# Optimization experiments

Measured on AMD Instinct MI355X. Metric: run time of the kernel, lower is better.

Reference implementation:

```python
import jax, jax.numpy as jnp
import numpy as np

NUM_HEADS = 8
HEAD_DIM = 32
ATTN_DIM = NUM_HEADS * HEAD_DIM  # 256
WINDOW_SIZES = (7, 5)
DILATIONS = (1, 2)
SCALE_FACTORS = (2, 4)


def conv1x1(x, W, b):
    # x: [B, C, H, W], W: [O, C], b: [O]
    return jnp.einsum('bchw,oc->bohw', x, W) + b[None, :, None, None]


def gather_neighbors(x, window, dilation):
    """Zero-padded dilated neighborhood gather.
    x: [B, C, h, w] -> neighbors [B, C, K, h, w], valid mask [K, h, w] (K = window**2)."""
    B, C, h, w = x.shape
    pad = dilation * (window // 2)
    xp = jnp.pad(x, ((0, 0), (0, 0), (pad, pad), (pad, pad)))
    mp = jnp.pad(jnp.ones((h, w), dtype=bool), ((pad, pad), (pad, pad)))
    neigh, masks = [], []
    for i in range(window):
        for j in range(window):
            dy, dx = dilation * i, dilation * j
            neigh.append(xp[:, :, dy:dy + h, dx:dx + w])
            masks.append(mp[dy:dy + h, dx:dx + w])
    return jnp.stack(neigh, axis=2), jnp.stack(masks, axis=0)


def align_to_query_grid(t, Hq, Wq, sf):
    """Repeat coarse-lattice candidates onto the fine query grid via anchor indexing."""
    y = jnp.minimum(jnp.arange(Hq) // sf, t.shape[-2] - 1)
    x = jnp.minimum(jnp.arange(Wq) // sf, t.shape[-1] - 1)
    return jnp.take(jnp.take(t, y, axis=-2), x, axis=-1)


def _forward(query, mems, Wq, bq, Wks, bks, Wvs, bvs, Wfuse, bfuse):
    B, _, Hq, Wq_ = query.shape
    q = conv1x1(query, Wq, bq)                                  # [B, attn, Hq, Wq]
    qh = q.reshape(B, NUM_HEADS, HEAD_DIM, Hq, Wq_)             # [B, n, d, H, W]
    scale = HEAD_DIM ** -0.5
    outs = []
    for s, mem in enumerate(mems):
        k = conv1x1(mem, Wks[s], bks[s])                        # [B, attn, hm, wm]
        v = conv1x1(mem, Wvs[s], bvs[s])
        kn, mask = gather_neighbors(k, WINDOW_SIZES[s], DILATIONS[s])  # [B, attn, K, hm, wm]
        vn, _ = gather_neighbors(v, WINDOW_SIZES[s], DILATIONS[s])
        K = kn.shape[2]
        hm, wm = kn.shape[-2:]
        kn = kn.reshape(B, NUM_HEADS, HEAD_DIM, K, hm, wm).transpose(0, 1, 3, 2, 4, 5)  # [B,n,K,d,hm,wm]
        vn = vn.reshape(B, NUM_HEADS, HEAD_DIM, K, hm, wm).transpose(0, 1, 3, 2, 4, 5)
        kn = align_to_query_grid(kn, Hq, Wq_, SCALE_FACTORS[s])  # [B,n,K,d,Hq,Wq]
        vn = align_to_query_grid(vn, Hq, Wq_, SCALE_FACTORS[s])
        mask_f = align_to_query_grid(mask, Hq, Wq_, SCALE_FACTORS[s])  # [K,Hq,Wq]
        scores = jnp.einsum('bndhw,bnkdhw->bnkhw', qh, kn) * scale
        neg = jnp.finfo(scores.dtype).min
        scores = jnp.where(mask_f[None, None], scores, neg)
        attn = jax.nn.softmax(scores, axis=2)                    # over K candidates
        o = jnp.einsum('bnkhw,bnkdhw->bndhw', attn, vn)
        outs.append(o.reshape(B, ATTN_DIM, Hq, Wq_))
    fused = jnp.concatenate(outs, axis=1)                        # [B, S*attn, Hq, Wq]
    return conv1x1(fused, Wfuse, bfuse)                          # [B, attn, Hq, Wq]


def setup_inputs() -> dict:
    key = jax.random.key(0)
    ks = jax.random.split(key, 16)
    std = 0.02
    inp = {
        'query': jax.random.normal(ks[0], (2, 256, 64, 64), jnp.float32),
        'mem0': jax.random.normal(ks[1], (2, 384, 32, 32), jnp.float32),
        'mem1': jax.random.normal(ks[2], (2, 768, 16, 16), jnp.float32),
        'Wq': jax.random.normal(ks[3], (ATTN_DIM, 256), jnp.float32) * std,
        'bq': jnp.zeros((ATTN_DIM,), jnp.float32),
        'Wk0': jax.random.normal(ks[4], (ATTN_DIM, 384), jnp.float32) * std,
        'bk0': jnp.zeros((ATTN_DIM,), jnp.float32),
        'Wv0': jax.random.normal(ks[5], (ATTN_DIM, 384), jnp.float32) * std,
        'bv0': jnp.zeros((ATTN_DIM,), jnp.float32),
        'Wk1': jax.random.normal(ks[6], (ATTN_DIM, 768), jnp.float32) * std,
        'bk1': jnp.zeros((ATTN_DIM,), jnp.float32),
        'Wv1': jax.random.normal(ks[7], (ATTN_DIM, 768), jnp.float32) * std,
        'bv1': jnp.zeros((ATTN_DIM,), jnp.float32),
        'Wfuse': jax.random.normal(ks[8], (ATTN_DIM, 2 * ATTN_DIM), jnp.float32) * std,
        'bfuse': jnp.zeros((ATTN_DIM,), jnp.float32),
    }
    return inp


def reference(query, mem0, mem1, Wq, bq, Wk0, bk0, Wv0, bv0, Wk1, bk1, Wv1, bv1, Wfuse, bfuse):
    return _forward(query, (mem0, mem1), Wq, bq, (Wk0, Wk1), (bk0, bk1), (Wv0, Wv1), (bv0, bv1), Wfuse, bfuse)
```

## Files before the change

kernel.cpp:

```cpp
#include <hip/hip_runtime.h>
#include <math.h>

typedef unsigned short u16;
typedef unsigned int u32;
typedef __attribute__((ext_vector_type(8))) short bf16x8;
typedef __attribute__((ext_vector_type(4))) float f32x4;

__device__ __forceinline__ u16 f2bf(float x) {
    u32 b = __builtin_bit_cast(u32, x);
    b += 0x7FFFu + ((b >> 16) & 1u);
    return (u16)(b >> 16);
}
__device__ __forceinline__ float bf2f(u16 u) {
    u32 b = ((u32)u) << 16;
    return __builtin_bit_cast(float, b);
}

__device__ __forceinline__ size_t sw_unit(int row, int c, int CC) {
    int slot = (c & 63) >> 3;
    return ((size_t)((row >> 7) * CC + (c >> 6)) << 10)
         + (size_t)((row & 127) << 3) + (size_t)(slot ^ (row & 7));
}

__device__ void prep_x(const float* __restrict__ X, int C, int HW, int bl, int PT,
                       u16* __restrict__ dh) {
    __shared__ float Xt[64][65];
    const int t = threadIdx.x;
    const int pt = bl % PT, ct = bl / PT;
    const int p0 = pt * 64, c0 = ct * 64;
    const int b = p0 / HW, hw0 = p0 % HW;
    #pragma unroll
    for (int i = 0; i < 16; i++) {
        int r = (t >> 6) + i * 4;
        Xt[r][t & 63] = X[(size_t)(b * C + c0 + r) * HW + hw0 + (t & 63)];
    }
    __syncthreads();
    const int CC = C >> 6;
    #pragma unroll
    for (int it = 0; it < 2; it++) {
        int id = t + it * 256;
        int px = id >> 3, sl = id & 7;
        bf16x8 hv;
        #pragma unroll
        for (int j = 0; j < 8; j++)
            hv[j] = (short)f2bf(Xt[sl * 8 + j][px]);
        size_t unit = sw_unit(p0 + px, c0 + sl * 8, CC);
        *(bf16x8*)(dh + unit * 8) = hv;
    }
}

__device__ void prep_w(const float* __restrict__ W, int C, int bl,
                       u16* __restrict__ dh, u16* __restrict__ dl, bool wlo) {
    const int t = threadIdx.x;
    const int ot = bl & 3, cc = bl >> 2;
    const int o0 = ot * 64, c0 = cc * 64;
    const int CC = C >> 6;
    #pragma unroll
    for (int it = 0; it < 2; it++) {
        int id = t + it * 256;
        int ol = id >> 3, sl = id & 7;
        int o = o0 + ol, c = c0 + sl * 8;
        const float* wp = W + (size_t)o * C + c;
        float4 a = *(const float4*)wp;
        float4 b2 = *(const float4*)(wp + 4);
        float xs[8] = {a.x, a.y, a.z, a.w, b2.x, b2.y, b2.z, b2.w};
        bf16x8 hv, lv;
        #pragma unroll
        for (int j = 0; j < 8; j++) {
            u16 h = f2bf(xs[j]);
            hv[j] = (short)h;
            lv[j] = (short)f2bf(xs[j] - bf2f(h));
        }
        size_t unit = sw_unit(o, c, CC);
        *(bf16x8*)(dh + unit * 8) = hv;
        if (wlo) *(bf16x8*)(dl + unit * 8) = lv;
    }
}

#define OFF_WQ 0
#define OFF_WK0 65536
#define OFF_WV0 163840
#define OFF_WK1 262144
#define OFF_WV1 458752
#define OFF_WFUSE 655360

__global__ __launch_bounds__(256) void prep_k(
    const float* __restrict__ query, const float* __restrict__ mem0, const float* __restrict__ mem1,
    const float* __restrict__ Wq, const float* __restrict__ Wk0, const float* __restrict__ Wv0,
    const float* __restrict__ Wk1, const float* __restrict__ Wv1, const float* __restrict__ Wfuse,
    u16* Xq_hi, u16* Xm0_hi, u16* Xm1_hi, u16* Whi, u16* Wlo)
{
    const int bx = blockIdx.x;
    if (bx < 512)      prep_x(query, 256, 4096, bx,       128, Xq_hi);
    else if (bx < 704) prep_x(mem0,  384, 1024, bx - 512,  32, Xm0_hi);
    else if (bx < 800) prep_x(mem1,  768,  256, bx - 704,   8, Xm1_hi);
    else {
        int r = bx - 800;
        if (r < 16)       prep_w(Wq,    256, r,       Whi + OFF_WQ,    Wlo, false);
        else if (r < 40)  prep_w(Wk0,   384, r - 16,  Whi + OFF_WK0,   Wlo, false);
        else if (r < 64)  prep_w(Wv0,   384, r - 40,  Whi + OFF_WV0,   Wlo, false);
        else if (r < 112) prep_w(Wk1,   768, r - 64,  Whi + OFF_WK1,   Wlo, false);
        else if (r < 160) prep_w(Wv1,   768, r - 112, Whi + OFF_WV1,   Wlo, false);
        else              prep_w(Wfuse, 512, r - 160, Whi + OFF_WFUSE, Wlo + OFF_WFUSE, true);
    }
}

template<int TERMS, bool OUT16>
__device__ __forceinline__ void gemm_core(
    const u16* __restrict__ Ahi, const u16* __restrict__ Alo,
    const u16* __restrict__ Bhi, const float* __restrict__ bias,
    void* __restrict__ Y, int CC, int am, int bn, u16* smem)
{
    const int t = threadIdx.x, lane = t & 63, w = t >> 6;
    const int wr = w >> 1, wc = w & 1;
    const int l15 = lane & 15;

    f32x4 acc[4][4];
    #pragma unroll
    for (int a = 0; a < 4; a++)
        #pragma unroll
        for (int b2 = 0; b2 < 4; b2++)
            acc[a][b2] = (f32x4){0.f, 0.f, 0.f, 0.f};

    bf16x8 stg[TERMS + 1][4];
    {
        const size_t aoff = ((size_t)(am * CC)) << 13;
        const size_t boff = ((size_t)(bn * CC)) << 13;
        #pragma unroll
        for (int it = 0; it < 4; it++) {
            const size_t o = (size_t)(t + it * 256) * 8;
            stg[0][it] = *(const bf16x8*)(Ahi + aoff + o);
            if constexpr (TERMS == 2) stg[1][it] = *(const bf16x8*)(Alo + aoff + o);
            stg[TERMS][it] = *(const bf16x8*)(Bhi + boff + o);
        }
    }

    for (int ck = 0; ck < CC; ck++) {
        __syncthreads();
        #pragma unroll
        for (int p = 0; p <= TERMS; p++)
            #pragma unroll
            for (int it = 0; it < 4; it++)
                *(bf16x8*)(smem + p * 8192 + (size_t)(t + it * 256) * 8) = stg[p][it];
        __syncthreads();

        {
            const int cn = (ck + 1 < CC) ? ck + 1 : ck;
            const size_t aoff = ((size_t)(am * CC + cn)) << 13;
            const size_t boff = ((size_t)(bn * CC + cn)) << 13;
            #pragma unroll
            for (int it = 0; it < 4; it++) {
                const size_t o = (size_t)(t + it * 256) * 8;
                stg[0][it] = *(const bf16x8*)(Ahi + aoff + o);
                if constexpr (TERMS == 2) stg[1][it] = *(const bf16x8*)(Alo + aoff + o);
                stg[TERMS][it] = *(const bf16x8*)(Bhi + boff + o);
            }
        }

        #pragma unroll
        for (int kk = 0; kk < 2; kk++) {
            bf16x8 ah[4], al[4], bh[4];
            #pragma unroll
            for (int tr = 0; tr < 4; tr++) {
                int row = wr * 64 + tr * 16 + l15;
                int off = row * 64 + (((kk * 4 + (lane >> 4)) ^ (row & 7)) << 3);
                ah[tr] = *(const bf16x8*)(smem + off);
                if constexpr (TERMS == 2) al[tr] = *(const bf16x8*)(smem + 8192 + off);
            }
            #pragma unroll
            for (int tc = 0; tc < 4; tc++) {
                int row = wc * 64 + tc * 16 + l15;
                int off = row * 64 + (((kk * 4 + (lane >> 4)) ^ (row & 7)) << 3);
                bh[tc] = *(const bf16x8*)(smem + TERMS * 8192 + off);
            }
            #pragma unroll
            for (int tr = 0; tr < 4; tr++)
                #pragma unroll
                for (int tc = 0; tc < 4; tc++) {
                    acc[tr][tc] = __builtin_amdgcn_mfma_f32_16x16x32_bf16(ah[tr], bh[tc], acc[tr][tc], 0, 0, 0);
                    if constexpr (TERMS == 2)
                        acc[tr][tc] = __builtin_amdgcn_mfma_f32_16x16x32_bf16(al[tr], bh[tc], acc[tr][tc], 0, 0, 0);
                }
        }
    }

    if (OUT16) {
        u16* Y16 = (u16*)Y;
        float bv[4];
        #pragma unroll
        for (int tc = 0; tc < 4; tc++)
            bv[tc] = bias[bn * 128 + wc * 64 + tc * 16 + l15];
        #pragma unroll
        for (int tr = 0; tr < 4; tr++) {
            #pragma unroll
            for (int i = 0; i < 4; i++) {
                int rp = am * 128 + wr * 64 + tr * 16 + ((lane >> 4) << 2) + i;
                u16* yr = Y16 + (size_t)rp * 256 + bn * 128 + wc * 64 + l15;
                #pragma unroll
                for (int tc = 0; tc < 4; tc++)
                    yr[tc * 16] = f2bf(acc[tr][tc][i] + bv[tc]);
            }
        }
    } else {
        float* Yf = (float*)Y;
        #pragma unroll
        for (int tr = 0; tr < 4; tr++) {
            #pragma unroll
            for (int i = 0; i < 4; i++) {
                int o = am * 128 + wr * 64 + tr * 16 + ((lane >> 4) << 2) + i;
                float bv = bias[o];
                #pragma unroll
                for (int tc = 0; tc < 4; tc++) {
                    int pcol = bn * 128 + wc * 64 + tc * 16 + l15;
                    Yf[(size_t)((pcol >> 12) * 256 + o) * 4096 + (pcol & 4095)] = acc[tr][tc][i] + bv;
                }
            }
        }
    }
}

__global__ __launch_bounds__(256) void projmm_k(
    const u16* __restrict__ Xq_hi, const u16* __restrict__ Xm0_hi,
    const u16* __restrict__ Xm1_hi, const u16* __restrict__ Whi,
    const float* __restrict__ bq, const float* __restrict__ bk0, const float* __restrict__ bv0,
    const float* __restrict__ bk1, const float* __restrict__ bv1,
    u16* qT, u16* k0T, u16* v0T, u16* k1T, u16* v1T)
{
    __shared__ u16 smem[16384];
    const int bx = blockIdx.x;
    if (bx < 128) {
        gemm_core<1, true>(Xq_hi, nullptr, Whi + OFF_WQ, bq, (void*)qT, 4, bx >> 1, bx & 1, smem);
    } else if (bx < 192) {
        const int r = bx - 128, am = r >> 2, bnn = r & 3;
        if (bnn < 2) gemm_core<1, true>(Xm0_hi, nullptr, Whi + OFF_WK0, bk0, (void*)k0T, 6, am, bnn, smem);
        else         gemm_core<1, true>(Xm0_hi, nullptr, Whi + OFF_WV0, bv0, (void*)v0T, 6, am, bnn - 2, smem);
    } else {
        const int r = bx - 192, am = r >> 2, bnn = r & 3;
        if (bnn < 2) gemm_core<1, true>(Xm1_hi, nullptr, Whi + OFF_WK1, bk1, (void*)k1T, 12, am, bnn, smem);
        else         gemm_core<1, true>(Xm1_hi, nullptr, Whi + OFF_WV1, bv1, (void*)v1T, 12, am, bnn - 2, smem);
    }
}

__global__ __launch_bounds__(256) void fusemm_k(
    const u16* __restrict__ Whi, const u16* __restrict__ Wlo,
    const u16* __restrict__ fhi, const float* __restrict__ bfuse, float* out)
{
    __shared__ u16 smem[24576];
    const int bx = blockIdx.x;
    gemm_core<2, false>(Whi + OFF_WFUSE, Wlo + OFF_WFUSE, fhi, bfuse, (void*)out,
                        8, bx & 1, bx >> 1, smem);
}

template<int SCALE>
__device__ __forceinline__ void attn_mfma(
    const u16* __restrict__ qT, const u16* __restrict__ kT,
    const u16* __restrict__ vT, u16* __restrict__ fhi,
    int b, int n, int ty, int tx, int lane, u16* s_lds)
{
    constexpr int HM = SCALE ? 16 : 32;
    const int qy0 = ty * 4, qx0 = tx * 4;
    const int ay0 = SCALE ? (qy0 >> 2) : (qy0 >> 1);
    const int ax0 = SCALE ? (qx0 >> 2) : (qx0 >> 1);
    const int l15 = lane & 15, kg = lane >> 4;

    const int pA = (b * 64 + qy0 + (l15 >> 2)) * 64 + qx0 + (l15 & 3);
    const bf16x8 qf = *(const bf16x8*)(qT + (size_t)pA * 256 + n * 32 + kg * 8);

    f32x4 s[4];
    #pragma unroll
    for (int t = 0; t < 4; t++) {
        const int cand = t * 16 + l15;
        const int wy = cand >> 3, wx = cand & 7;
        const int my = SCALE ? (ay0 + (wy - 2) * 2) : (ay0 - 3 + wy);
        const int mx = SCALE ? (ax0 + (wx - 2) * 2) : (ax0 - 3 + wx);
        const int myc = min(max(my, 0), HM - 1), mxc = min(max(mx, 0), HM - 1);
        const bf16x8 kf = *(const bf16x8*)(kT + (size_t)((b * HM + myc) * HM + mxc) * 256 + n * 32 + kg * 8);
        s[t] = __builtin_amdgcn_mfma_f32_16x16x32_bf16(qf, kf, (f32x4){0.f, 0.f, 0.f, 0.f}, 0, 0, 0);
    }

    const float scl = 0.17677669529663687f;
    float sv[4][4];
    #pragma unroll
    for (int t = 0; t < 4; t++) {
        const int cand = t * 16 + l15;
        const int wy = cand >> 3, wx = cand & 7;
        const int my = SCALE ? (ay0 + (wy - 2) * 2) : (ay0 - 3 + wy);
        const int mx = SCALE ? (ax0 + (wx - 2) * 2) : (ax0 - 3 + wx);
        const bool inb = (my >= 0) && (my < HM) && (mx >= 0) && (mx < HM);
        #pragma unroll
        for (int i = 0; i < 4; i++) {
            bool ok;
            if (SCALE) {
                ok = inb && (wy < 5) && (wx < 5);
            } else {
                const int r = kg * 4 + i;
                const int dy2 = (r >> 2) >> 1, dx2 = (r & 3) >> 1;
                ok = inb && ((u32)(wy - dy2) <= 6u) && ((u32)(wx - dx2) <= 6u);
            }
            sv[t][i] = ok ? s[t][i] * scl : -1e30f;
        }
    }

    float linv[4];
    #pragma unroll
    for (int i = 0; i < 4; i++) {
        float m = fmaxf(fmaxf(sv[0][i], sv[1][i]), fmaxf(sv[2][i], sv[3][i]));
        #pragma unroll
        for (int dd = 1; dd < 16; dd <<= 1) m = fmaxf(m, __shfl_xor(m, dd, 64));
        float l = 0.f;
        #pragma unroll
        for (int t = 0; t < 4; t++) { sv[t][i] = __expf(sv[t][i] - m); l += sv[t][i]; }
        #pragma unroll
        for (int dd = 1; dd < 16; dd <<= 1) l += __shfl_xor(l, dd, 64);
        linv[i] = 1.f / l;
    }

    #pragma unroll
    for (int t = 0; t < 4; t++)
        #pragma unroll
        for (int i = 0; i < 4; i++)
            s_lds[(kg * 4 + i) * 68 + t * 16 + l15] = f2bf(sv[t][i]);
    __syncthreads();

    f32x4 o[2] = {(f32x4){0.f,0.f,0.f,0.f}, (f32x4){0.f,0.f,0.f,0.f}};
    #pragma unroll
    for (int h = 0; h < 2; h++) {
        const bf16x8 pa = *(const bf16x8*)(s_lds + l15 * 68 + h * 32 + kg * 8);
        #pragma unroll
        for (int c = 0; c < 2; c++) {
            bf16x8 vf;
            #pragma unroll
            for (int j = 0; j < 8; j++) {
                const int cand = h * 32 + kg * 8 + j;
                const int wy = cand >> 3, wx = cand & 7;
                int my = SCALE ? (ay0 + (wy - 2) * 2) : (ay0 - 3 + wy);
                int mx = SCALE ? (ax0 + (wx - 2) * 2) : (ax0 - 3 + wx);
                my = min(max(my, 0), HM - 1); mx = min(max(mx, 0), HM - 1);
                vf[j] = (short)vT[(size_t)((b * HM + my) * HM + mx) * 256 + n * 32 + c * 16 + l15];
            }
            o[c] = __builtin_amdgcn_mfma_f32_16x16x32_bf16(pa, vf, o[c], 0, 0, 0);
        }
    }

    #pragma unroll
    for (int c = 0; c < 2; c++) {
        #pragma unroll
        for (int i = 0; i < 4; i++) {
            const int r = kg * 4 + i;
            const int p = (b * 64 + qy0 + (r >> 2)) * 64 + qx0 + (r & 3);
            const int ch = (SCALE ? 256 : 0) + n * 32 + c * 16 + l15;
            fhi[sw_unit(p, ch, 8) * 8 + (ch & 7)] = f2bf(o[c][i] * linv[i]);
        }
    }
}

__global__ __launch_bounds__(256) void attn_k(
    const u16* __restrict__ qT,
    const u16* __restrict__ k0T, const u16* __restrict__ v0T,
    const u16* __restrict__ k1T, const u16* __restrict__ v1T,
    u16* __restrict__ fhi)
{
    __shared__ u16 s_lds[4][16 * 68];
    const int t = threadIdx.x, w = t >> 6, lane = t & 63;
    const int bx = blockIdx.x;
    const int sc = bx >> 10;
    const int tile = (bx & 1023) * 4 + w;
    const int b = tile >> 11, n = (tile >> 8) & 7;
    const int ty = (tile >> 4) & 15, tx = tile & 15;
    if (sc == 0) attn_mfma<0>(qT, k0T, v0T, fhi, b, n, ty, tx, lane, s_lds[w]);
    else         attn_mfma<1>(qT, k1T, v1T, fhi, b, n, ty, tx, lane, s_lds[w]);
}

extern "C" void kernel_launch(void* const* d_in, const int* in_sizes, int n_in,
                              void* d_out, int out_size, void* d_ws, size_t ws_size,
                              hipStream_t stream)
{
    const float* query = (const float*)d_in[0];
    const float* mem0  = (const float*)d_in[1];
    const float* mem1  = (const float*)d_in[2];
    const float* Wq    = (const float*)d_in[3];  const float* bq    = (const float*)d_in[4];
    const float* Wk0   = (const float*)d_in[5];  const float* bk0   = (const float*)d_in[6];
    const float* Wv0   = (const float*)d_in[7];  const float* bv0   = (const float*)d_in[8];
    const float* Wk1   = (const float*)d_in[9];  const float* bk1   = (const float*)d_in[10];
    const float* Wv1   = (const float*)d_in[11]; const float* bv1   = (const float*)d_in[12];
    const float* Wfuse = (const float*)d_in[13]; const float* bfuse = (const float*)d_in[14];
    float* out = (float*)d_out;

    char* ws = (char*)d_ws;
    u16* qT       = (u16*)(ws + 0);
    u16* k0T      = (u16*)(ws + 8388608);
    u16* v0T      = (u16*)(ws + 10485760);
    u16* k1T      = (u16*)(ws + 12582912);
    u16* v1T      = (u16*)(ws + 13107200);
    u16* Whi      = (u16*)(ws + 13631488);
    u16* Wlo      = (u16*)(ws + 15204352);
    u16* Xm0_hi   = (u16*)(ws + 16777216);
    u16* Xm1_hi   = (u16*)(ws + 19922944);
    u16* Xq_hi    = (u16*)(ws + 21495808);
    u16* fhi      = Xq_hi;

    prep_k<<<dim3(992), 256, 0, stream>>>(
        query, mem0, mem1, Wq, Wk0, Wv0, Wk1, Wv1, Wfuse,
        Xq_hi, Xm0_hi, Xm1_hi, Whi, Wlo);

    projmm_k<<<dim3(208), 256, 0, stream>>>(
        Xq_hi, Xm0_hi, Xm1_hi, Whi,
        bq, bk0, bv0, bk1, bv1, qT, k0T, v0T, k1T, v1T);

    attn_k<<<dim3(2048), 256, 0, stream>>>(qT, k0T, v0T, k1T, v1T, fhi);

    fusemm_k<<<dim3(128), 256, 0, stream>>>(Whi, Wlo, fhi, bfuse, out);
}
```

Baseline: 56.04 us.

## Drop split-bf16 low term in fuse GEMM and retile it to 64-row blocks

The fuse projection no longer uses a hi/lo split of the weights, so it runs one bf16 MFMA per tile instead of two and stops loading and storing the low-part weights. The fuse GEMM also becomes its own kernel with 64x128 output tiles and 256 blocks instead of 128, to fill more compute units and use less LDS per block. This lowers the accuracy of the final projection, which now runs at plain bf16 precision and may come closer to the tolerance limit.

```diff
diff --git a/kernel.cpp b/kernel.cpp
--- a/kernel.cpp
+++ b/kernel.cpp
@@ -50,7 +50,7 @@
 }
 
 __device__ void prep_w(const float* __restrict__ W, int C, int bl,
-                       u16* __restrict__ dh, u16* __restrict__ dl, bool wlo) {
+                       u16* __restrict__ dh) {
     const int t = threadIdx.x;
     const int ot = bl & 3, cc = bl >> 2;
     const int o0 = ot * 64, c0 = cc * 64;
@@ -64,16 +64,12 @@
         float4 a = *(const float4*)wp;
         float4 b2 = *(const float4*)(wp + 4);
         float xs[8] = {a.x, a.y, a.z, a.w, b2.x, b2.y, b2.z, b2.w};
-        bf16x8 hv, lv;
-        #pragma unroll
-        for (int j = 0; j < 8; j++) {
-            u16 h = f2bf(xs[j]);
-            hv[j] = (short)h;
-            lv[j] = (short)f2bf(xs[j] - bf2f(h));
-        }
+        bf16x8 hv;
+        #pragma unroll
+        for (int j = 0; j < 8; j++)
+            hv[j] = (short)f2bf(xs[j]);
         size_t unit = sw_unit(o, c, CC);
         *(bf16x8*)(dh + unit * 8) = hv;
-        if (wlo) *(bf16x8*)(dl + unit * 8) = lv;
     }
 }
 
@@ -88,7 +84,7 @@
     const float* __restrict__ query, const float* __restrict__ mem0, const float* __restrict__ mem1,
     const float* __restrict__ Wq, const float* __restrict__ Wk0, const float* __restrict__ Wv0,
     const float* __restrict__ Wk1, const float* __restrict__ Wv1, const float* __restrict__ Wfuse,
-    u16* Xq_hi, u16* Xm0_hi, u16* Xm1_hi, u16* Whi, u16* Wlo)
+    u16* Xq_hi, u16* Xm0_hi, u16* Xm1_hi, u16* Whi)
 {
     const int bx = blockIdx.x;
     if (bx < 512)      prep_x(query, 256, 4096, bx,       128, Xq_hi);
@@ -96,20 +92,19 @@
     else if (bx < 800) prep_x(mem1,  768,  256, bx - 704,   8, Xm1_hi);
     else {
         int r = bx - 800;
-        if (r < 16)       prep_w(Wq,    256, r,       Whi + OFF_WQ,    Wlo, false);
-        else if (r < 40)  prep_w(Wk0,   384, r - 16,  Whi + OFF_WK0,   Wlo, false);
-        else if (r < 64)  prep_w(Wv0,   384, r - 40,  Whi + OFF_WV0,   Wlo, false);
-        else if (r < 112) prep_w(Wk1,   768, r - 64,  Whi + OFF_WK1,   Wlo, false);
-        else if (r < 160) prep_w(Wv1,   768, r - 112, Whi + OFF_WV1,   Wlo, false);
-        else              prep_w(Wfuse, 512, r - 160, Whi + OFF_WFUSE, Wlo + OFF_WFUSE, true);
-    }
-}
-
-template<int TERMS, bool OUT16>
+        if (r < 16)       prep_w(Wq,    256, r,       Whi + OFF_WQ);
+        else if (r < 40)  prep_w(Wk0,   384, r - 16,  Whi + OFF_WK0);
+        else if (r < 64)  prep_w(Wv0,   384, r - 40,  Whi + OFF_WV0);
+        else if (r < 112) prep_w(Wk1,   768, r - 64,  Whi + OFF_WK1);
+        else if (r < 160) prep_w(Wv1,   768, r - 112, Whi + OFF_WV1);
+        else              prep_w(Wfuse, 512, r - 160, Whi + OFF_WFUSE);
+    }
+}
+
 __device__ __forceinline__ void gemm_core(
-    const u16* __restrict__ Ahi, const u16* __restrict__ Alo,
-    const u16* __restrict__ Bhi, const float* __restrict__ bias,
-    void* __restrict__ Y, int CC, int am, int bn, u16* smem)
+    const u16* __restrict__ Ahi, const u16* __restrict__ Bhi,
+    const float* __restrict__ bias, u16* __restrict__ Y,
+    int CC, int am, int bn, u16* smem)
 {
     const int t = threadIdx.x, lane = t & 63, w = t >> 6;
     const int wr = w >> 1, wc = w & 1;
@@ -122,7 +117,7 @@
         for (int b2 = 0; b2 < 4; b2++)
             acc[a][b2] = (f32x4){0.f, 0.f, 0.f, 0.f};
 
-    bf16x8 stg[TERMS + 1][4];
+    bf16x8 stg[2][4];
     {
         const size_t aoff = ((size_t)(am * CC)) << 13;
         const size_t boff = ((size_t)(bn * CC)) << 13;
@@ -130,15 +125,14 @@
         for (int it = 0; it < 4; it++) {
             const size_t o = (size_t)(t + it * 256) * 8;
             stg[0][it] = *(const bf16x8*)(Ahi + aoff + o);
-            if constexpr (TERMS == 2) stg[1][it] = *(const bf16x8*)(Alo + aoff + o);
-            stg[TERMS][it] = *(const bf16x8*)(Bhi + boff + o);
+            stg[1][it] = *(const bf16x8*)(Bhi + boff + o);
         }
     }
 
     for (int ck = 0; ck < CC; ck++) {
         __syncthreads();
         #pragma unroll
-        for (int p = 0; p <= TERMS; p++)
+        for (int p = 0; p < 2; p++)
             #pragma unroll
             for (int it = 0; it < 4; it++)
                 *(bf16x8*)(smem + p * 8192 + (size_t)(t + it * 256) * 8) = stg[p][it];
@@ -152,69 +146,46 @@
             for (int it = 0; it < 4; it++) {
                 const size_t o = (size_t)(t + it * 256) * 8;
                 stg[0][it] = *(const bf16x8*)(Ahi + aoff + o);
-                if constexpr (TERMS == 2) stg[1][it] = *(const bf16x8*)(Alo + aoff + o);
-                stg[TERMS][it] = *(const bf16x8*)(Bhi + boff + o);
+                stg[1][it] = *(const bf16x8*)(Bhi + boff + o);
             }
         }
 
         #pragma unroll
         for (int kk = 0; kk < 2; kk++) {
-            bf16x8 ah[4], al[4], bh[4];
+            bf16x8 ah[4], bh[4];
             #pragma unroll
             for (int tr = 0; tr < 4; tr++) {
                 int row = wr * 64 + tr * 16 + l15;
                 int off = row * 64 + (((kk * 4 + (lane >> 4)) ^ (row & 7)) << 3);
                 ah[tr] = *(const bf16x8*)(smem + off);
-                if constexpr (TERMS == 2) al[tr] = *(const bf16x8*)(smem + 8192 + off);
             }
             #pragma unroll
             for (int tc = 0; tc < 4; tc++) {
                 int row = wc * 64 + tc * 16 + l15;
                 int off = row * 64 + (((kk * 4 + (lane >> 4)) ^ (row & 7)) << 3);
-                bh[tc] = *(const bf16x8*)(smem + TERMS * 8192 + off);
+                bh[tc] = *(const bf16x8*)(smem + 8192 + off);
             }
             #pragma unroll
             for (int tr = 0; tr < 4; tr++)
                 #pragma unroll
-                for (int tc = 0; tc < 4; tc++) {
+                for (int tc = 0; tc < 4; tc++)
                     acc[tr][tc] = __builtin_amdgcn_mfma_f32_16x16x32_bf16(ah[tr], bh[tc], acc[tr][tc], 0, 0, 0);
-                    if constexpr (TERMS == 2)
-                        acc[tr][tc] = __builtin_amdgcn_mfma_f32_16x16x32_bf16(al[tr], bh[tc], acc[tr][tc], 0, 0, 0);
-                }
-        }
-    }
-
-    if (OUT16) {
-        u16* Y16 = (u16*)Y;
-        float bv[4];
-        #pragma unroll
-        for (int tc = 0; tc < 4; tc++)
-            bv[tc] = bias[bn * 128 + wc * 64 + tc * 16 + l15];
-        #pragma unroll
-        for (int tr = 0; tr < 4; tr++) {
-            #pragma unroll
-            for (int i = 0; i < 4; i++) {
-                int rp = am * 128 + wr * 64 + tr * 16 + ((lane >> 4) << 2) + i;
-                u16* yr = Y16 + (size_t)rp * 256 + bn * 128 + wc * 64 + l15;
-                #pragma unroll
-                for (int tc = 0; tc < 4; tc++)
-                    yr[tc * 16] = f2bf(acc[tr][tc][i] + bv[tc]);
-            }
-        }
-    } else {
-        float* Yf = (float*)Y;
-        #pragma unroll
-        for (int tr = 0; tr < 4; tr++) {
-            #pragma unroll
-            for (int i = 0; i < 4; i++) {
-                int o = am * 128 + wr * 64 + tr * 16 + ((lane >> 4) << 2) + i;
-                float bv = bias[o];
-                #pragma unroll
-                for (int tc = 0; tc < 4; tc++) {
-                    int pcol = bn * 128 + wc * 64 + tc * 16 + l15;
-                    Yf[(size_t)((pcol >> 12) * 256 + o) * 4096 + (pcol & 4095)] = acc[tr][tc][i] + bv;
-                }
-            }
+        }
+    }
+
+    float bv[4];
+    #pragma unroll
+    for (int tc = 0; tc < 4; tc++)
+        bv[tc] = bias[bn * 128 + wc * 64 + tc * 16 + l15];
+    #pragma unroll
+    for (int tr = 0; tr < 4; tr++) {
+        #pragma unroll
+        for (int i = 0; i < 4; i++) {
+            int rp = am * 128 + wr * 64 + tr * 16 + ((lane >> 4) << 2) + i;
+            u16* yr = Y + (size_t)rp * 256 + bn * 128 + wc * 64 + l15;
+            #pragma unroll
+            for (int tc = 0; tc < 4; tc++)
+                yr[tc * 16] = f2bf(acc[tr][tc][i] + bv[tc]);
         }
     }
 }
@@ -229,26 +200,106 @@
     __shared__ u16 smem[16384];
     const int bx = blockIdx.x;
     if (bx < 128) {
-        gemm_core<1, true>(Xq_hi, nullptr, Whi + OFF_WQ, bq, (void*)qT, 4, bx >> 1, bx & 1, smem);
+        gemm_core(Xq_hi, Whi + OFF_WQ, bq, qT, 4, bx >> 1, bx & 1, smem);
     } else if (bx < 192) {
         const int r = bx - 128, am = r >> 2, bnn = r & 3;
-        if (bnn < 2) gemm_core<1, true>(Xm0_hi, nullptr, Whi + OFF_WK0, bk0, (void*)k0T, 6, am, bnn, smem);
-        else         gemm_core<1, true>(Xm0_hi, nullptr, Whi + OFF_WV0, bv0, (void*)v0T, 6, am, bnn - 2, smem);
+        if (bnn < 2) gemm_core(Xm0_hi, Whi + OFF_WK0, bk0, k0T, 6, am, bnn, smem);
+        else         gemm_core(Xm0_hi, Whi + OFF_WV0, bv0, v0T, 6, am, bnn - 2, smem);
     } else {
         const int r = bx - 192, am = r >> 2, bnn = r & 3;
-        if (bnn < 2) gemm_core<1, true>(Xm1_hi, nullptr, Whi + OFF_WK1, bk1, (void*)k1T, 12, am, bnn, smem);
-        else         gemm_core<1, true>(Xm1_hi, nullptr, Whi + OFF_WV1, bv1, (void*)v1T, 12, am, bnn - 2, smem);
+        if (bnn < 2) gemm_core(Xm1_hi, Whi + OFF_WK1, bk1, k1T, 12, am, bnn, smem);
+        else         gemm_core(Xm1_hi, Whi + OFF_WV1, bv1, v1T, 12, am, bnn - 2, smem);
     }
 }
 
 __global__ __launch_bounds__(256) void fusemm_k(
-    const u16* __restrict__ Whi, const u16* __restrict__ Wlo,
-    const u16* __restrict__ fhi, const float* __restrict__ bfuse, float* out)
-{
-    __shared__ u16 smem[24576];
-    const int bx = blockIdx.x;
-    gemm_core<2, false>(Whi + OFF_WFUSE, Wlo + OFF_WFUSE, fhi, bfuse, (void*)out,
-                        8, bx & 1, bx >> 1, smem);
+    const u16* __restrict__ Whi, const u16* __restrict__ fhi,
+    const float* __restrict__ bias, float* __restrict__ out)
+{
+    __shared__ u16 smem[12288];
+    const int t = threadIdx.x, lane = t & 63, w = t >> 6;
+    const int wr = w >> 1, wc = w & 1;
+    const int l15 = lane & 15;
+    const int am = blockIdx.x & 3, bn = blockIdx.x >> 2;
+    const u16* A = Whi + OFF_WFUSE;
+
+    f32x4 acc[2][4];
+    #pragma unroll
+    for (int a = 0; a < 2; a++)
+        #pragma unroll
+        for (int b2 = 0; b2 < 4; b2++)
+            acc[a][b2] = (f32x4){0.f, 0.f, 0.f, 0.f};
+
+    bf16x8 stgA[2], stgB[4];
+    {
+        const size_t aoff = (((size_t)(am >> 1) * 8) << 10) + (size_t)(am & 1) * 512;
+        const size_t boff = ((size_t)(bn * 8)) << 10;
+        #pragma unroll
+        for (int it = 0; it < 2; it++)
+            stgA[it] = *(const bf16x8*)(A + (aoff + t + it * 256) * 8);
+        #pragma unroll
+        for (int it = 0; it < 4; it++)
+            stgB[it] = *(const bf16x8*)(fhi + (boff + t + it * 256) * 8);
+    }
+
+    for (int ck = 0; ck < 8; ck++) {
+        __syncthreads();
+        #pragma unroll
+        for (int it = 0; it < 2; it++)
+            *(bf16x8*)(smem + (size_t)(t + it * 256) * 8) = stgA[it];
+        #pragma unroll
+        for (int it = 0; it < 4; it++)
+            *(bf16x8*)(smem + 4096 + (size_t)(t + it * 256) * 8) = stgB[it];
+        __syncthreads();
+
+        {
+            const int cn = (ck + 1 < 8) ? ck + 1 : ck;
+            const size_t aoff = (((size_t)(am >> 1) * 8 + cn) << 10) + (size_t)(am & 1) * 512;
+            const size_t boff = ((size_t)(bn * 8 + cn)) << 10;
+            #pragma unroll
+            for (int it = 0; it < 2; it++)
+                stgA[it] = *(const bf16x8*)(A + (aoff + t + it * 256) * 8);
+            #pragma unroll
+            for (int it = 0; it < 4; it++)
+                stgB[it] = *(const bf16x8*)(fhi + (boff + t + it * 256) * 8);
+        }
+
+        #pragma unroll
+        for (int kk = 0; kk < 2; kk++) {
+            bf16x8 ah[2], bh[4];
+            #pragma unroll
+            for (int tr = 0; tr < 2; tr++) {
+                int row = wr * 32 + tr * 16 + l15;
+                int off = row * 64 + (((kk * 4 + (lane >> 4)) ^ (row & 7)) << 3);
+                ah[tr] = *(const bf16x8*)(smem + off);
+            }
+            #pragma unroll
+            for (int tc = 0; tc < 4; tc++) {
+                int row = wc * 64 + tc * 16 + l15;
+                int off = row * 64 + (((kk * 4 + (lane >> 4)) ^ (row & 7)) << 3);
+                bh[tc] = *(const bf16x8*)(smem + 4096 + off);
+            }
+            #pragma unroll
+            for (int tr = 0; tr < 2; tr++)
+                #pragma unroll
+                for (int tc = 0; tc < 4; tc++)
+                    acc[tr][tc] = __builtin_amdgcn_mfma_f32_16x16x32_bf16(ah[tr], bh[tc], acc[tr][tc], 0, 0, 0);
+        }
+    }
+
+    #pragma unroll
+    for (int tr = 0; tr < 2; tr++) {
+        #pragma unroll
+        for (int i = 0; i < 4; i++) {
+            const int o = am * 64 + wr * 32 + tr * 16 + ((lane >> 4) << 2) + i;
+            const float bv = bias[o];
+            #pragma unroll
+            for (int tc = 0; tc < 4; tc++) {
+                const int pcol = bn * 128 + wc * 64 + tc * 16 + l15;
+                out[(size_t)((pcol >> 12) * 256 + o) * 4096 + (pcol & 4095)] = acc[tr][tc][i] + bv;
+            }
+        }
+    }
 }
 
 template<int SCALE>
@@ -393,7 +444,6 @@
     u16* k1T      = (u16*)(ws + 12582912);
     u16* v1T      = (u16*)(ws + 13107200);
     u16* Whi      = (u16*)(ws + 13631488);
-    u16* Wlo      = (u16*)(ws + 15204352);
     u16* Xm0_hi   = (u16*)(ws + 16777216);
     u16* Xm1_hi   = (u16*)(ws + 19922944);
     u16* Xq_hi    = (u16*)(ws + 21495808);
@@ -401,7 +451,7 @@
 
     prep_k<<<dim3(992), 256, 0, stream>>>(
         query, mem0, mem1, Wq, Wk0, Wv0, Wk1, Wv1, Wfuse,
-        Xq_hi, Xm0_hi, Xm1_hi, Whi, Wlo);
+        Xq_hi, Xm0_hi, Xm1_hi, Whi);
 
     projmm_k<<<dim3(208), 256, 0, stream>>>(
         Xq_hi, Xm0_hi, Xm1_hi, Whi,
@@ -409,5 +459,5 @@
 
     attn_k<<<dim3(2048), 256, 0, stream>>>(qT, k0T, v0T, k1T, v1T, fhi);
 
-    fusemm_k<<<dim3(128), 256, 0, stream>>>(Whi, Wlo, fhi, bfuse, out);
-}
+    fusemm_k<<<dim3(256), 256, 0, stream>>>(Whi, fhi, bfuse, out);
+}
```

Result: faster. 50.21 us (-10.4%).
